# Performance work log

Measured on AMD Instinct MI355X. Metric: run time of the kernel, lower is better.

The kernel has to match this reference:

```python
import jax, jax.numpy as jnp
import numpy as np

D = 2048
B = 8192

def setup_inputs() -> dict:
    key = jax.random.key(0)
    ks = jax.random.split(key, 11)
    s = 1.0 / np.sqrt(D)  # torch Linear default init scale
    return {
        "e_t": jax.random.normal(ks[0], (B, D), dtype=jnp.float32),
        "h_prev": jax.random.normal(ks[1], (B, 2 * D), dtype=jnp.float32),
        "W_p": jax.random.uniform(ks[2], (D, D), jnp.float32, -s, s),
        "b_p": jax.random.uniform(ks[3], (D,), jnp.float32, -s, s),
        "W_theta": jax.random.uniform(ks[4], (D, D), jnp.float32, -s, s),
        "b_theta": jax.random.uniform(ks[5], (D,), jnp.float32, -s, s),
        "W_r": jax.random.uniform(ks[6], (D, D), jnp.float32, -s, s),
        "b_r": jax.random.uniform(ks[7], (D,), jnp.float32, -s, s),
        "W_i": jax.random.uniform(ks[8], (D, D), jnp.float32, -s, s),
        "b_i": jax.random.uniform(ks[9], (D,), jnp.float32, -s, s),
    }

def reference(e_t, h_prev, W_p, b_p, W_theta, b_theta, W_r, b_r, W_i, b_i):
    d = e_t.shape[-1]
    # fuse the four projections into one GEMM: [B, D] @ [D, 4D]
    W_cat = jnp.concatenate([W_p, W_theta, W_r, W_i], axis=0)  # torch Linear: y = x @ W.T + b
    b_cat = jnp.concatenate([b_p, b_theta, b_r, b_i], axis=0)
    proj = e_t @ W_cat.T + b_cat  # [B, 4D]
    p_lin, theta_t, inp_re, inp_im = jnp.split(proj, 4, axis=-1)
    p_t = jax.nn.sigmoid(p_lin)
    cos_t = jnp.cos(theta_t)
    sin_t = jnp.sin(theta_t)
    h_re = h_prev[:, :d]
    h_im = h_prev[:, d:]
    rot_re = cos_t * h_re - sin_t * h_im
    rot_im = sin_t * h_re + cos_t * h_im
    new_re = (1 - p_t) * rot_re + p_t * inp_re
    new_im = (1 - p_t) * rot_im + p_t * inp_im
    return jnp.concatenate([new_re, new_im], axis=-1)
```

## Files before the change

kernel.cpp:

```cpp
#include <hip/hip_runtime.h>


typedef float f32x16 __attribute__((ext_vector_type(16)));
typedef __bf16 bf16x8 __attribute__((ext_vector_type(8)));
typedef short short8 __attribute__((ext_vector_type(8)));

__device__ __forceinline__ unsigned short f2bf(float f) {
    unsigned u = __float_as_uint(f);
    u += 0x7fffu + ((u >> 16) & 1u);
    return (unsigned short)(u >> 16);
}

__global__ __launch_bounds__(256) void cvt_all(
    const float* __restrict__ W_p, const float* __restrict__ W_th,
    const float* __restrict__ W_r, const float* __restrict__ W_i,
    const float* __restrict__ e_t,
    unsigned short* __restrict__ Wbf, unsigned short* __restrict__ Ebf) {
    const long i = (long)blockIdx.x * 256 + threadIdx.x;
    const float* src;
    unsigned short* dst;
    size_t local;
    if (i < 2097152) {
        const int m = (int)(i >> 19);
        local = (size_t)(i & 524287) * 8;
        src = (m == 0) ? W_p : (m == 1) ? W_th : (m == 2) ? W_r : W_i;
        dst = Wbf + (size_t)m * 4194304 + local;
    } else {
        local = (size_t)(i - 2097152) * 8;
        src = e_t;
        dst = Ebf + local;
    }
    const float4* s4 = (const float4*)(src + local);
    float4 v0 = s4[0], v1 = s4[1];
    ushort4 o0, o1;
    o0.x = f2bf(v0.x); o0.y = f2bf(v0.y); o0.z = f2bf(v0.z); o0.w = f2bf(v0.w);
    o1.x = f2bf(v1.x); o1.y = f2bf(v1.y); o1.z = f2bf(v1.z); o1.w = f2bf(v1.w);
    ((ushort4*)dst)[0] = o0;
    ((ushort4*)dst)[1] = o1;
}

__device__ __forceinline__ void load16_lds(const unsigned short* g, unsigned short* l) {
    __builtin_amdgcn_global_load_lds((const __attribute__((address_space(1))) void*)g,
                                     (__attribute__((address_space(3))) void*)l,
                                     16, 0, 0);
}

__device__ __forceinline__ bf16x8 ldfrag(const unsigned short* p) {
    return __builtin_bit_cast(bf16x8, *(const short8*)p);
}

__global__ __launch_bounds__(256, 2) void mipt_main(
    const unsigned short* __restrict__ E,
    const unsigned short* __restrict__ W,
    const float* __restrict__ b_p, const float* __restrict__ b_th,
    const float* __restrict__ b_r, const float* __restrict__ b_i,
    const float* __restrict__ h_prev,
    float* __restrict__ out)
{
    __shared__ unsigned short As[256 * 32];
    __shared__ unsigned short Bs[128 * 32];

    const int tid  = threadIdx.x;
    const int wave = tid >> 6;
    const int lane = tid & 63;
    const int m0 = blockIdx.x * 256;
    const int n0 = blockIdx.y * 32;

    f32x16 acc[2][4];
#pragma unroll
    for (int i = 0; i < 2; ++i)
#pragma unroll
        for (int j = 0; j < 4; ++j)
#pragma unroll
            for (int r = 0; r < 16; ++r) acc[i][j][r] = 0.f;

    const int srow = lane >> 2;
    const int scol = ((lane & 3) ^ ((lane >> 3) & 3)) * 8;
    const unsigned short* Ag = E + (size_t)(m0 + wave * 64 + srow) * 2048 + scol;
    unsigned short* Al = As + (wave * 64) * 32;
    const unsigned short* Bg = W + (size_t)(wave * 2048 + n0 + srow) * 2048 + scol;
    unsigned short* Bl = Bs + (wave * 32) * 32;

    const int L  = lane & 31;
    const int hi = lane >> 5;
    const int sw = (L >> 1) & 3;
    const int s0off = (hi ^ sw) * 8;
    const int s1off = ((hi ^ 2) ^ sw) * 8;
    const unsigned short* ApL = As + (size_t)(wave * 64 + L) * 32;
    const unsigned short* BpL = Bs + (size_t)L * 32;

#pragma unroll 1
    for (int kt = 0; kt < 64; ++kt) {
        const int k0 = kt * 32;
#pragma unroll
        for (int j = 0; j < 4; ++j) load16_lds(Ag + (size_t)j * 16 * 2048 + k0, Al + j * 16 * 32);
#pragma unroll
        for (int j = 0; j < 2; ++j) load16_lds(Bg + (size_t)j * 16 * 2048 + k0, Bl + j * 16 * 32);
        __syncthreads();

        bf16x8 a[2][2], b[4][2];
#pragma unroll
        for (int ti = 0; ti < 2; ++ti) {
            a[ti][0] = ldfrag(ApL + ti * 32 * 32 + s0off);
            a[ti][1] = ldfrag(ApL + ti * 32 * 32 + s1off);
        }
#pragma unroll
        for (int tj = 0; tj < 4; ++tj) {
            b[tj][0] = ldfrag(BpL + tj * 32 * 32 + s0off);
            b[tj][1] = ldfrag(BpL + tj * 32 * 32 + s1off);
        }

#pragma unroll
        for (int tj = 0; tj < 4; ++tj)
#pragma unroll
            for (int ti = 0; ti < 2; ++ti)
                acc[ti][tj] = __builtin_amdgcn_mfma_f32_32x32x16_bf16(a[ti][0], b[tj][0], acc[ti][tj], 0, 0, 0);
#pragma unroll
        for (int tj = 0; tj < 4; ++tj)
#pragma unroll
            for (int ti = 0; ti < 2; ++ti)
                acc[ti][tj] = __builtin_amdgcn_mfma_f32_32x32x16_bf16(a[ti][1], b[tj][1], acc[ti][tj], 0, 0, 0);
        __syncthreads();
    }

    const int col = n0 + L;
    const float bp = b_p[col], bt = b_th[col], br = b_r[col], bi = b_i[col];
    const int rowb = m0 + wave * 64 + 4 * hi;
#pragma unroll
    for (int ti = 0; ti < 2; ++ti) {
#pragma unroll
        for (int r = 0; r < 16; ++r) {
            const int row = rowb + ti * 32 + (r & 3) + 8 * (r >> 2);
            const float pl  = acc[ti][0][r] + bp;
            const float th  = acc[ti][1][r] + bt;
            const float ire = acc[ti][2][r] + br;
            const float iim = acc[ti][3][r] + bi;
            const float p = 1.f / (1.f + __expf(-pl));
            float s, ct;
            __sincosf(th, &s, &ct);
            const size_t base = (size_t)row * 4096 + col;
            const float hre = h_prev[base];
            const float him = h_prev[base + 2048];
            const float rre = ct * hre - s * him;
            const float rim = s * hre + ct * him;
            out[base]        = (1.f - p) * rre + p * ire;
            out[base + 2048] = (1.f - p) * rim + p * iim;
        }
    }
}

extern "C" void kernel_launch(void* const* d_in, const int* in_sizes, int n_in,
                              void* d_out, int out_size, void* d_ws, size_t ws_size,
                              hipStream_t stream) {
    (void)in_sizes; (void)n_in; (void)out_size; (void)ws_size;
    const float* e_t   = (const float*)d_in[0];
    const float* h_prv = (const float*)d_in[1];
    const float* W_p   = (const float*)d_in[2];
    const float* b_p   = (const float*)d_in[3];
    const float* W_th  = (const float*)d_in[4];
    const float* b_th  = (const float*)d_in[5];
    const float* W_r   = (const float*)d_in[6];
    const float* b_r   = (const float*)d_in[7];
    const float* W_i   = (const float*)d_in[8];
    const float* b_i   = (const float*)d_in[9];
    float* out = (float*)d_out;

    unsigned short* Wbf = (unsigned short*)d_ws;
    unsigned short* Ebf = Wbf + (size_t)8192 * 2048;

    cvt_all<<<16384, 256, 0, stream>>>(W_p, W_th, W_r, W_i, e_t, Wbf, Ebf);

    dim3 grid(32, 64);
    mipt_main<<<grid, 256, 0, stream>>>(Ebf, Wbf, b_p, b_th, b_r, b_i, h_prv, out);
}
```

Before: 596.6 us.

## Double-buffer LDS with BK=64, 8-wave 256x64 tiles and swizzled block order

```diff
diff --git a/kernel.cpp b/kernel.cpp
--- a/kernel.cpp
+++ b/kernel.cpp
@@ -49,7 +49,7 @@
     return __builtin_bit_cast(bf16x8, *(const short8*)p);
 }
 
-__global__ __launch_bounds__(256, 2) void mipt_main(
+__global__ __launch_bounds__(512, 2) void mipt_main(
     const unsigned short* __restrict__ E,
     const unsigned short* __restrict__ W,
     const float* __restrict__ b_p, const float* __restrict__ b_th,
@@ -57,14 +57,19 @@
     const float* __restrict__ h_prev,
     float* __restrict__ out)
 {
-    __shared__ unsigned short As[256 * 32];
-    __shared__ unsigned short Bs[128 * 32];
+    __shared__ unsigned short As[2 * 256 * 64];
+    __shared__ unsigned short Bs[2 * 256 * 64];
 
     const int tid  = threadIdx.x;
-    const int wave = tid >> 6;
+    const int w    = tid >> 6;
     const int lane = tid & 63;
-    const int m0 = blockIdx.x * 256;
-    const int n0 = blockIdx.y * 32;
+    const int wr   = w >> 1;
+    const int wc   = w & 1;
+
+    const int bid = (int)blockIdx.x;
+    const int swz = (bid & 7) * 128 + (bid >> 3);
+    const int m0 = (swz & 31) * 256;
+    const int n0 = (swz >> 5) * 64;
 
     f32x16 acc[2][4];
 #pragma unroll
@@ -74,58 +79,80 @@
 #pragma unroll
             for (int r = 0; r < 16; ++r) acc[i][j][r] = 0.f;
 
-    const int srow = lane >> 2;
-    const int scol = ((lane & 3) ^ ((lane >> 3) & 3)) * 8;
-    const unsigned short* Ag = E + (size_t)(m0 + wave * 64 + srow) * 2048 + scol;
-    unsigned short* Al = As + (wave * 64) * 32;
-    const unsigned short* Bg = W + (size_t)(wave * 2048 + n0 + srow) * 2048 + scol;
-    unsigned short* Bl = Bs + (wave * 32) * 32;
+    const int sr = lane >> 3;
+    const int sc = ((lane & 7) ^ sr) * 8;
+    const unsigned short* Ag = E + (size_t)(m0 + w * 32 + sr) * 2048 + sc;
+    const unsigned short* Bg = W + (size_t)(wr * 2048 + n0 + wc * 32 + sr) * 2048 + sc;
+    const int dA = w * 2048;
 
     const int L  = lane & 31;
     const int hi = lane >> 5;
-    const int sw = (L >> 1) & 3;
-    const int s0off = (hi ^ sw) * 8;
-    const int s1off = ((hi ^ 2) ^ sw) * 8;
-    const unsigned short* ApL = As + (size_t)(wave * 64 + L) * 32;
-    const unsigned short* BpL = Bs + (size_t)L * 32;
+    const int r7 = L & 7;
+    const int aoff = (wr * 64 + L) * 64;
+    const int boff = (wc * 32 + L) * 64;
+
+#pragma unroll
+    for (int j = 0; j < 4; ++j) {
+        load16_lds(Ag + (size_t)(j * 8) * 2048, As + dA + j * 512);
+        load16_lds(Bg + (size_t)(j * 8) * 2048, Bs + dA + j * 512);
+    }
+    asm volatile("s_waitcnt vmcnt(0)" ::: "memory");
+    __builtin_amdgcn_s_barrier();
 
 #pragma unroll 1
-    for (int kt = 0; kt < 64; ++kt) {
-        const int k0 = kt * 32;
-#pragma unroll
-        for (int j = 0; j < 4; ++j) load16_lds(Ag + (size_t)j * 16 * 2048 + k0, Al + j * 16 * 32);
-#pragma unroll
-        for (int j = 0; j < 2; ++j) load16_lds(Bg + (size_t)j * 16 * 2048 + k0, Bl + j * 16 * 32);
-        __syncthreads();
-
-        bf16x8 a[2][2], b[4][2];
-#pragma unroll
-        for (int ti = 0; ti < 2; ++ti) {
-            a[ti][0] = ldfrag(ApL + ti * 32 * 32 + s0off);
-            a[ti][1] = ldfrag(ApL + ti * 32 * 32 + s1off);
+    for (int t = 0; t < 32; ++t) {
+        const int so = (t & 1) << 14;
+        const int sn = so ^ 16384;
+        const bool pf = (t < 31);
+        const unsigned short* Agt = Ag + (size_t)(t + 1) * 64;
+        const unsigned short* Bgt = Bg + (size_t)(t + 1) * 64;
+        const unsigned short* aC = As + so + aoff;
+        const unsigned short* bC = Bs + so + boff;
+        unsigned short* dAn = As + sn + dA;
+        unsigned short* dBn = Bs + sn + dA;
+
+#pragma unroll
+        for (int q = 0; q < 4; ++q) {
+            if (pf) {
+                if (q == 0) {
+                    load16_lds(Agt,                 dAn);
+                    load16_lds(Bgt,                 dBn);
+                    load16_lds(Agt + (size_t)8 * 2048,  dAn + 512);
+                    load16_lds(Bgt + (size_t)8 * 2048,  dBn + 512);
+                } else if (q == 1) {
+                    load16_lds(Agt + (size_t)16 * 2048, dAn + 1024);
+                    load16_lds(Bgt + (size_t)16 * 2048, dBn + 1024);
+                } else if (q == 2) {
+                    load16_lds(Agt + (size_t)24 * 2048, dAn + 1536);
+                    load16_lds(Bgt + (size_t)24 * 2048, dBn + 1536);
+                }
+            }
+            const int qo = ((2 * q + hi) ^ r7) * 8;
+            bf16x8 a0 = ldfrag(aC + qo);
+            bf16x8 a1 = ldfrag(aC + 2048 + qo);
+            bf16x8 b0 = ldfrag(bC + qo);
+            bf16x8 b1 = ldfrag(bC + 4096 + qo);
+            bf16x8 b2 = ldfrag(bC + 8192 + qo);
+            bf16x8 b3 = ldfrag(bC + 12288 + qo);
+            __builtin_amdgcn_s_barrier();
+            __builtin_amdgcn_s_setprio(1);
+            acc[0][0] = __builtin_amdgcn_mfma_f32_32x32x16_bf16(a0, b0, acc[0][0], 0, 0, 0);
+            acc[1][0] = __builtin_amdgcn_mfma_f32_32x32x16_bf16(a1, b0, acc[1][0], 0, 0, 0);
+            acc[0][1] = __builtin_amdgcn_mfma_f32_32x32x16_bf16(a0, b1, acc[0][1], 0, 0, 0);
+            acc[1][1] = __builtin_amdgcn_mfma_f32_32x32x16_bf16(a1, b1, acc[1][1], 0, 0, 0);
+            acc[0][2] = __builtin_amdgcn_mfma_f32_32x32x16_bf16(a0, b2, acc[0][2], 0, 0, 0);
+            acc[1][2] = __builtin_amdgcn_mfma_f32_32x32x16_bf16(a1, b2, acc[1][2], 0, 0, 0);
+            acc[0][3] = __builtin_amdgcn_mfma_f32_32x32x16_bf16(a0, b3, acc[0][3], 0, 0, 0);
+            acc[1][3] = __builtin_amdgcn_mfma_f32_32x32x16_bf16(a1, b3, acc[1][3], 0, 0, 0);
+            __builtin_amdgcn_s_setprio(0);
+            if (q == 3 && pf) asm volatile("s_waitcnt vmcnt(0)" ::: "memory");
+            __builtin_amdgcn_s_barrier();
         }
-#pragma unroll
-        for (int tj = 0; tj < 4; ++tj) {
-            b[tj][0] = ldfrag(BpL + tj * 32 * 32 + s0off);
-            b[tj][1] = ldfrag(BpL + tj * 32 * 32 + s1off);
-        }
-
-#pragma unroll
-        for (int tj = 0; tj < 4; ++tj)
-#pragma unroll
-            for (int ti = 0; ti < 2; ++ti)
-                acc[ti][tj] = __builtin_amdgcn_mfma_f32_32x32x16_bf16(a[ti][0], b[tj][0], acc[ti][tj], 0, 0, 0);
-#pragma unroll
-        for (int tj = 0; tj < 4; ++tj)
-#pragma unroll
-            for (int ti = 0; ti < 2; ++ti)
-                acc[ti][tj] = __builtin_amdgcn_mfma_f32_32x32x16_bf16(a[ti][1], b[tj][1], acc[ti][tj], 0, 0, 0);
-        __syncthreads();
-    }
-
-    const int col = n0 + L;
+    }
+
+    const int col = n0 + wc * 32 + L;
     const float bp = b_p[col], bt = b_th[col], br = b_r[col], bi = b_i[col];
-    const int rowb = m0 + wave * 64 + 4 * hi;
+    const int rowb = m0 + wr * 64 + 4 * hi;
 #pragma unroll
     for (int ti = 0; ti < 2; ++ti) {
 #pragma unroll
@@ -170,6 +197,5 @@
 
     cvt_all<<<16384, 256, 0, stream>>>(W_p, W_th, W_r, W_i, e_t, Wbf, Ebf);
 
-    dim3 grid(32, 64);
-    mipt_main<<<grid, 256, 0, stream>>>(Ebf, Wbf, b_p, b_th, b_r, b_i, h_prv, out);
-}
+    mipt_main<<<1024, 512, 0, stream>>>(Ebf, Wbf, b_p, b_th, b_r, b_i, h_prv, out);
+}
```

Result: slower. 741.8 us (+24.3%).
